# Optimization experiments

Measured on AMD Instinct MI355X. Metric: run time of the kernel, lower is better.

## Reference

```python
import jax, jax.numpy as jnp
import numpy as np

N, F, B, D = 16384, 256, 48, 8


def setup_inputs() -> dict:
    key = jax.random.key(0)
    k_x, k_e, k_w, k_b = jax.random.split(key, 4)
    x = jax.random.normal(k_x, (N, F), dtype=jnp.float32)
    # per-feature sorted bin boundaries -> left edges and positive widths
    boundaries = jnp.sort(jax.random.uniform(k_e, (F, B + 1), dtype=jnp.float32,
                                             minval=-3.0, maxval=3.0), axis=-1)
    edges = boundaries[:, :-1]                     # [F, B]
    width = jnp.diff(boundaries, axis=-1)          # [F, B], > 0
    bound = 1.0 / np.sqrt(B)                       # nn.Linear default init
    W = jax.random.uniform(k_w, (F, B, D), dtype=jnp.float32, minval=-bound, maxval=bound)
    b = jax.random.uniform(k_b, (F, D), dtype=jnp.float32, minval=-bound, maxval=bound)
    return {"x": x, "edges": edges, "width": width, "W": W, "b": b}


def reference(x, edges, width, W, b):
    # piecewise-linear encoding: [N, F, B]
    h = (x[:, :, None] - edges) / width
    h = jnp.concatenate([
        jnp.minimum(h[..., :1], 1.0),          # first bin: clamp_max(1)
        jnp.clip(h[..., 1:-1], 0.0, 1.0),      # middle bins: clamp(0, 1)
        jnp.maximum(h[..., -1:], 0.0),         # last bin: clamp_min(0)
    ], axis=-1)
    # per-feature tiny Linear(B -> D), then concat over features
    out = jnp.einsum('nfb,fbd->nfd', h, W) + b   # [N, F, D]
    return out.reshape(x.shape[0], -1)           # [N, F*D]
```

## Files before the change

### kernel.cpp

```cpp
#include <hip/hip_runtime.h>


#define NN 16384
#define FF 256
#define BB 48
#define DD 8

#define FT 16
#define NSPLIT 128
#define NPB (NN / NSPLIT)

#define ESTR 17
#define CSTR (49 * DD + 4)

__global__ __launch_bounds__(256, 5)
void cple_kernel(const float* __restrict__ X,
                 const float* __restrict__ Edg,
                 const float* __restrict__ Wid,
                 const float* __restrict__ W,
                 const float* __restrict__ Bias,
                 float* __restrict__ Out)
{
    __shared__ float sE[49 * ESTR];
    __shared__ float sR[48 * ESTR];
    __shared__ float sC[FT * CSTR];

    const int tid = threadIdx.x;
    const int f0  = blockIdx.x * FT;
    const int ns  = blockIdx.y;

    {
        const float4* Wt4 = (const float4*)(W + (size_t)f0 * BB * DD);
        for (int idx4 = tid; idx4 < FT * BB * DD / 4; idx4 += 256) {
            float4 v = Wt4[idx4];
            int idx = idx4 * 4;
            int f   = idx / (BB * DD);
            int rem = idx - f * (BB * DD);
            int b   = rem >> 3;
            int d   = rem & 7;
            float* dst = &sC[f * CSTR + (b + 1) * DD + d];
            dst[0] = v.x; dst[1] = v.y; dst[2] = v.z; dst[3] = v.w;
        }
    }
    for (int idx = tid; idx < FT * BB; idx += 256) {
        int f = idx / BB;
        int j = idx - f * BB;
        sE[j * ESTR + f] = Edg[(size_t)(f0 + f) * BB + j];
        sR[j * ESTR + f] = 1.0f / Wid[(size_t)(f0 + f) * BB + j];
    }
    if (tid < FT) sE[48 * ESTR + tid] = __builtin_inff();
    __syncthreads();

    if (tid < FT * DD) {
        int f = tid >> 3;
        int d = tid & 7;
        float acc = Bias[(size_t)(f0 + f) * DD + d];
        float* c = &sC[f * CSTR + d];
        c[0] = acc;
        #pragma unroll
        for (int b = 1; b <= BB; ++b) {
            acc += c[b * DD];
            c[b * DD] = acc;
        }
    }
    __syncthreads();

    const int f_l  = tid & 15;
    const int n_l  = tid >> 4;
    const float* cF = &sC[f_l * CSTR];
    const int fcol = f0 + f_l;
    const float* xp = X + fcol;
    float* op = Out + (size_t)fcol * DD;

    const int n0 = ns * NPB + n_l;
    #pragma unroll
    for (int i = 0; i < NPB / 32; ++i) {
        int na = n0 + i * 32;
        int nb = na + 16;
        float xa = xp[(size_t)na * FF];
        float xb = xp[(size_t)nb * FF];

        int ka = 0, kb = 0;
        #pragma unroll
        for (int w = 32; w >= 1; w >>= 1) {
            ka += (xa >= sE[(ka + w) * ESTR + f_l]) ? w : 0;
            kb += (xb >= sE[(kb + w) * ESTR + f_l]) ? w : 0;
        }
        float ta = (xa - sE[ka * ESTR + f_l]) * sR[ka * ESTR + f_l];
        float tb = (xb - sE[kb * ESTR + f_l]) * sR[kb * ESTR + f_l];

        const float4* c4a = (const float4*)(cF + ka * DD);
        const float4* c4b = (const float4*)(cF + kb * DD);
        float4 a0 = c4a[0], a1 = c4a[1], a2 = c4a[2], a3 = c4a[3];
        float4 b0 = c4b[0], b1 = c4b[1], b2 = c4b[2], b3 = c4b[3];

        float4 oA0, oA1, oB0, oB1;
        oA0.x = fmaf(ta, a2.x - a0.x, a0.x);
        oA0.y = fmaf(ta, a2.y - a0.y, a0.y);
        oA0.z = fmaf(ta, a2.z - a0.z, a0.z);
        oA0.w = fmaf(ta, a2.w - a0.w, a0.w);
        oA1.x = fmaf(ta, a3.x - a1.x, a1.x);
        oA1.y = fmaf(ta, a3.y - a1.y, a1.y);
        oA1.z = fmaf(ta, a3.z - a1.z, a1.z);
        oA1.w = fmaf(ta, a3.w - a1.w, a1.w);
        oB0.x = fmaf(tb, b2.x - b0.x, b0.x);
        oB0.y = fmaf(tb, b2.y - b0.y, b0.y);
        oB0.z = fmaf(tb, b2.z - b0.z, b0.z);
        oB0.w = fmaf(tb, b2.w - b0.w, b0.w);
        oB1.x = fmaf(tb, b3.x - b1.x, b1.x);
        oB1.y = fmaf(tb, b3.y - b1.y, b1.y);
        oB1.z = fmaf(tb, b3.z - b1.z, b1.z);
        oB1.w = fmaf(tb, b3.w - b1.w, b1.w);

        float4* oa = (float4*)(op + (size_t)na * (FF * DD));
        float4* ob = (float4*)(op + (size_t)nb * (FF * DD));
        oa[0] = oA0; oa[1] = oA1;
        ob[0] = oB0; ob[1] = oB1;
    }
}

extern "C" void kernel_launch(void* const* d_in, const int* in_sizes, int n_in,
                              void* d_out, int out_size, void* d_ws, size_t ws_size,
                              hipStream_t stream) {
    const float* x     = (const float*)d_in[0];
    const float* edges = (const float*)d_in[1];
    const float* width = (const float*)d_in[2];
    const float* W     = (const float*)d_in[3];
    const float* b     = (const float*)d_in[4];
    float* out = (float*)d_out;

    dim3 grid(FF / FT, NSPLIT);
    cple_kernel<<<grid, 256, 0, stream>>>(x, edges, width, W, b, out);
}
```

Baseline: 164.5 us.

## Split each feature's output across two threads and halve the row split

Each thread now handles one row and half of a feature's 8 outputs (one float4). Thirty-two adjacent lanes cover 16 features × 8 outputs, which makes each warp's stores contiguous 512-byte runs. The row split per block is halved, so each block handles twice as many rows and the per-block setup (weight prefix sums) is amortised further. The binary search and edge lookup are now repeated by both threads of a feature pair, and occupancy hints drop from 5 to 4.

```diff
diff --git a/kernel.cpp b/kernel.cpp
--- a/kernel.cpp
+++ b/kernel.cpp
@@ -7,13 +7,13 @@
 #define DD 8
 
 #define FT 16
-#define NSPLIT 128
+#define NSPLIT 64
 #define NPB (NN / NSPLIT)
 
 #define ESTR 17
 #define CSTR (49 * DD + 4)
 
-__global__ __launch_bounds__(256, 5)
+__global__ __launch_bounds__(256, 4)
 void cple_kernel(const float* __restrict__ X,
                  const float* __restrict__ Edg,
                  const float* __restrict__ Wid,
@@ -65,57 +65,37 @@
     }
     __syncthreads();
 
-    const int f_l  = tid & 15;
-    const int n_l  = tid >> 4;
-    const float* cF = &sC[f_l * CSTR];
-    const int fcol = f0 + f_l;
+    const int slot = tid & 31;
+    const int f_l  = slot >> 1;
+    const int half = slot & 1;
+    const int r    = tid >> 5;
+
+    const float* cF = &sC[f_l * CSTR + half * 4];
+    const int fcol  = f0 + f_l;
     const float* xp = X + fcol;
-    float* op = Out + (size_t)fcol * DD;
+    float* op = Out + (size_t)f0 * DD + slot * 4;
 
-    const int n0 = ns * NPB + n_l;
-    #pragma unroll
-    for (int i = 0; i < NPB / 32; ++i) {
-        int na = n0 + i * 32;
-        int nb = na + 16;
-        float xa = xp[(size_t)na * FF];
-        float xb = xp[(size_t)nb * FF];
+    const int n0 = ns * NPB + r;
+    #pragma unroll 4
+    for (int i = 0; i < NPB / 8; ++i) {
+        int n = n0 + i * 8;
+        float x = xp[(size_t)n * FF];
 
-        int ka = 0, kb = 0;
+        int k = 0;
         #pragma unroll
-        for (int w = 32; w >= 1; w >>= 1) {
-            ka += (xa >= sE[(ka + w) * ESTR + f_l]) ? w : 0;
-            kb += (xb >= sE[(kb + w) * ESTR + f_l]) ? w : 0;
-        }
-        float ta = (xa - sE[ka * ESTR + f_l]) * sR[ka * ESTR + f_l];
-        float tb = (xb - sE[kb * ESTR + f_l]) * sR[kb * ESTR + f_l];
+        for (int w = 32; w >= 1; w >>= 1)
+            k += (x >= sE[(k + w) * ESTR + f_l]) ? w : 0;
+        float t = (x - sE[k * ESTR + f_l]) * sR[k * ESTR + f_l];
 
-        const float4* c4a = (const float4*)(cF + ka * DD);
-        const float4* c4b = (const float4*)(cF + kb * DD);
-        float4 a0 = c4a[0], a1 = c4a[1], a2 = c4a[2], a3 = c4a[3];
-        float4 b0 = c4b[0], b1 = c4b[1], b2 = c4b[2], b3 = c4b[3];
+        float4 lo = *(const float4*)(cF + k * DD);
+        float4 hi = *(const float4*)(cF + k * DD + DD);
+        float4 o;
+        o.x = fmaf(t, hi.x - lo.x, lo.x);
+        o.y = fmaf(t, hi.y - lo.y, lo.y);
+        o.z = fmaf(t, hi.z - lo.z, lo.z);
+        o.w = fmaf(t, hi.w - lo.w, lo.w);
 
-        float4 oA0, oA1, oB0, oB1;
-        oA0.x = fmaf(ta, a2.x - a0.x, a0.x);
-        oA0.y = fmaf(ta, a2.y - a0.y, a0.y);
-        oA0.z = fmaf(ta, a2.z - a0.z, a0.z);
-        oA0.w = fmaf(ta, a2.w - a0.w, a0.w);
-        oA1.x = fmaf(ta, a3.x - a1.x, a1.x);
-        oA1.y = fmaf(ta, a3.y - a1.y, a1.y);
-        oA1.z = fmaf(ta, a3.z - a1.z, a1.z);
-        oA1.w = fmaf(ta, a3.w - a1.w, a1.w);
-        oB0.x = fmaf(tb, b2.x - b0.x, b0.x);
-        oB0.y = fmaf(tb, b2.y - b0.y, b0.y);
-        oB0.z = fmaf(tb, b2.z - b0.z, b0.z);
-        oB0.w = fmaf(tb, b2.w - b0.w, b0.w);
-        oB1.x = fmaf(tb, b3.x - b1.x, b1.x);
-        oB1.y = fmaf(tb, b3.y - b1.y, b1.y);
-        oB1.z = fmaf(tb, b3.z - b1.z, b1.z);
-        oB1.w = fmaf(tb, b3.w - b1.w, b1.w);
-
-        float4* oa = (float4*)(op + (size_t)na * (FF * DD));
-        float4* ob = (float4*)(op + (size_t)nb * (FF * DD));
-        oa[0] = oA0; oa[1] = oA1;
-        ob[0] = oB0; ob[1] = oB1;
+        *(float4*)(op + (size_t)n * (FF * DD)) = o;
     }
 }
 
```

Result: slower. 193.7 us (+17.7%).
